# Optimization experiments

Hardware: AMD Instinct MI355X
Metric: run time of the kernel (lower is better)

Reference implementation:

```python
import jax, jax.numpy as jnp
import numpy as np

ALPHA_SCALE = 8.0  # exp(alpha_log_scale) where alpha_log_scale = log(8)
EPS = 1e-6


def _depthwise_causal_conv(x, conv_w, conv_b):
    # x: [N, H, T], conv_w: [H, 1, K], conv_b: [H]
    K = conv_w.shape[-1]
    y = jax.lax.conv_general_dilated(
        x, conv_w,
        window_strides=(1,),
        padding=[(K - 1, 0)],  # causal: torch pads both sides then slices [..., :T]
        dimension_numbers=("NCH", "OIH", "NCH"),
        feature_group_count=x.shape[1],
    )
    return y + conv_b[None, :, None]


def _linear_scan(alpha, x):
    # h_t = alpha_t * h_{t-1} + x_t along time axis=1; alpha, x: [N, T, H]
    def combine(c1, c2):
        a1, b1 = c1
        a2, b2 = c2
        return a1 * a2, a2 * b1 + b2
    _, h = jax.lax.associative_scan(combine, (alpha, x), axis=1)
    return h


def setup_inputs() -> dict:
    key = jax.random.key(0)
    ks = jax.random.split(key, 8)
    N, T, D = 4, 4096, 1024
    H, K = 1536, 4
    return {
        "x": jax.random.normal(ks[0], (N, T, D), dtype=jnp.float32),
        "W_in": jax.random.normal(ks[1], (2 * H, D), dtype=jnp.float32) * (D ** -0.5),
        "conv_w": jax.random.normal(ks[2], (H, 1, K), dtype=jnp.float32) * 0.1,
        "conv_b": jax.random.normal(ks[3], (H,), dtype=jnp.float32) * 0.1,
        "W_g": jax.random.normal(ks[4], (2 * H, H), dtype=jnp.float32) * (H ** -0.5),
        "b_g": jax.random.normal(ks[5], (2 * H,), dtype=jnp.float32) * 0.1,
        "forget_base": jax.random.normal(ks[6], (H,), dtype=jnp.float32),
        "W_out": jax.random.normal(ks[7], (D, H), dtype=jnp.float32) * (H ** -0.5),
    }


def reference(x, W_in, conv_w, conv_b, W_g, b_g, forget_base, W_out):
    H = W_g.shape[1]
    # input projection and split into gate / x branch
    gx = jnp.einsum("ntd,hd->nth", x, W_in)  # [N,T,2H]
    gate, xb = gx[..., :H], gx[..., H:]
    # depthwise causal conv
    xb = _depthwise_causal_conv(jnp.swapaxes(xb, 1, 2), conv_w, conv_b)
    xb = jnp.swapaxes(xb, 1, 2)  # [N,T,H]
    # gates
    fg = jnp.einsum("nth,gh->ntg", xb, W_g) + b_g  # [N,T,2H]
    forget, inp = fg[..., :H], fg[..., H:]
    # RG-LRU gating
    alpha = jnp.exp(-ALPHA_SCALE * jax.nn.softplus(forget_base) * jax.nn.sigmoid(forget))
    beta = jnp.sqrt(1.0 - alpha ** 2 + EPS)
    xs = beta * jax.nn.sigmoid(inp) * xb
    # linear recurrence h_t = alpha_t * h_{t-1} + xs_t
    h = _linear_scan(alpha, xs)
    # output projection with GeLU-gated hidden state (torch gelu = exact erf form)
    return jnp.einsum("nth,dh->ntd", jax.nn.gelu(gate, approximate=False) * h, W_out)
```

## Files before the change

### kernel.cpp

```cpp
#include <hip/hip_runtime.h>
#include <stdint.h>
#include <math.h>

#define N_B 4
#define T_S 4096
#define D_M 1024
#define H_M 1536
#define NT  (N_B * T_S)
#define G2  (2 * H_M)
#define LCH 64
#define NCH 64

typedef __attribute__((ext_vector_type(8))) short short8;
typedef __attribute__((ext_vector_type(4))) float floatx4;

__device__ __forceinline__ unsigned short f2bf(float f) {
  unsigned u = __float_as_uint(f);
  u += 0x7fff + ((u >> 16) & 1);
  return (unsigned short)(u >> 16);
}
__device__ __forceinline__ float bf2f(unsigned short u) {
  return __uint_as_float(((unsigned)u) << 16);
}
__device__ __forceinline__ float bf_lo(unsigned p) { return __uint_as_float(p << 16); }
__device__ __forceinline__ float bf_hi(unsigned p) { return __uint_as_float(p & 0xffff0000u); }
__device__ __forceinline__ unsigned bf_pack(float lo, float hi) {
  return ((unsigned)f2bf(lo)) | (((unsigned)f2bf(hi)) << 16);
}
__device__ __forceinline__ float sigmoidf_(float x) { return 1.f / (1.f + __expf(-x)); }
__device__ __forceinline__ float softplusf_(float x) {
  return (x > 20.f) ? x : log1pf(__expf(x));
}
__device__ __forceinline__ float geluf_(float x) {
  return 0.5f * x * (1.f + erff(x * 0.70710678118654752f));
}

__global__ void zero_out(float* __restrict__ out, int n) {
  int i = blockIdx.x * 256 + threadIdx.x;
  if (i < n) out[i] = 0.f;
}

#define N4_X   (NT * D_M / 4)
#define N4_WIN (G2 * D_M / 4)
#define N4_WG  (G2 * H_M / 4)
__global__ void cvt3_bf16(const float* __restrict__ x, unsigned short* __restrict__ x16,
                          const float* __restrict__ win, unsigned short* __restrict__ win16,
                          const float* __restrict__ wg, unsigned short* __restrict__ wg16) {
  int i = blockIdx.x * 256 + threadIdx.x;
  const float* in; unsigned short* out;
  if (i < N4_X)                { in = x;   out = x16; }
  else if (i < N4_X + N4_WIN)  { in = win; out = win16; i -= N4_X; }
  else if (i < N4_X + N4_WIN + N4_WG) { in = wg; out = wg16; i -= N4_X + N4_WIN; }
  else return;
  float4 v = ((const float4*)in)[i];
  ushort4 o;
  o.x = f2bf(v.x); o.y = f2bf(v.y); o.z = f2bf(v.z); o.w = f2bf(v.w);
  ((ushort4*)out)[i] = o;
}

__global__ void cvt_bf16(const float* __restrict__ in, unsigned short* __restrict__ out, int n4) {
  int i = blockIdx.x * 256 + threadIdx.x;
  if (i >= n4) return;
  float4 v = ((const float4*)in)[i];
  ushort4 o;
  o.x = f2bf(v.x); o.y = f2bf(v.y); o.z = f2bf(v.z); o.w = f2bf(v.w);
  ((ushort4*)out)[i] = o;
}

#define TM 256
#define TN 256

__device__ __forceinline__ void stage16(const unsigned short* g, unsigned short* l) {
  __builtin_amdgcn_global_load_lds((__attribute__((address_space(1))) void*)g,
                                   (__attribute__((address_space(3))) void*)l, 16, 0, 0);
}

template<bool BIAS, bool OUT_BF16, bool SPLIT>
__global__ __launch_bounds__(512, 2)
void gemm_bt8(const unsigned short* __restrict__ A,
              const unsigned short* __restrict__ B,
              void* __restrict__ Cv, void* __restrict__ Cv2,
              const float* __restrict__ bias,
              int N, int K) {
  __shared__ __align__(16) unsigned short lds[4][8192];
  const int tid  = threadIdx.x;
  const int lane = tid & 63;
  const int wave = tid >> 6;
  const int wr = wave >> 2;
  const int wc = wave & 3;

  const int gx  = gridDim.x;
  const int nwg = gx * gridDim.y;
  const int bid = blockIdx.y * gx + blockIdx.x;
  const int cpx = nwg >> 3;
  const int swz = (bid & 7) * cpx + (bid >> 3);
  const int bm = (swz / gx) * TM;
  const int bn = (swz % gx) * TN;

  floatx4 acc[8][4];
#pragma unroll
  for (int i = 0; i < 8; i++)
#pragma unroll
    for (int j = 0; j < 4; j++)
      acc[i][j] = (floatx4){0.f, 0.f, 0.f, 0.f};

  const int r0_ = tid >> 2;
  const int g8  = ((tid & 3) ^ ((tid >> 3) & 3)) * 8;
  const unsigned short* Ag1 = A + (size_t)(bm + r0_)       * K + g8;
  const unsigned short* Ag2 = A + (size_t)(bm + r0_ + 128) * K + g8;
  const unsigned short* Bg1 = B + (size_t)(bn + r0_)       * K + g8;
  const unsigned short* Bg2 = B + (size_t)(bn + r0_ + 128) * K + g8;
  const int ld1 = tid * 8;
  const int ld2 = ld1 + 4096;

#define STAGE_A(kh, kb) do { \
    stage16(Ag1 + (kb) + (kh) * 32, &lds[kh][ld1]); \
    stage16(Ag2 + (kb) + (kh) * 32, &lds[kh][ld2]); } while (0)
#define STAGE_B(kh, kb) do { \
    stage16(Bg1 + (kb) + (kh) * 32, &lds[2 + (kh)][ld1]); \
    stage16(Bg2 + (kb) + (kh) * 32, &lds[2 + (kh)][ld2]); } while (0)

  const int fr = lane & 15;
  const int kq = lane >> 4;
  const int sx = (kq ^ ((fr >> 1) & 3)) * 8;
  const int abase = (wr * 128 + fr) * 32 + sx;
  const int bbase = (wc * 64 + fr) * 32 + sx;

  const int nt = K >> 6;
  short8 af[8], bfr[2];

  STAGE_A(0, 0); STAGE_B(0, 0); STAGE_A(1, 0);

  for (int t = 0; t < nt; ++t) {
    const int k0 = t << 6;
    const int kn = k0 + 64;
    const bool st = (t + 1 < nt);

    STAGE_B(1, k0);
    asm volatile("s_waitcnt vmcnt(4)" ::: "memory");
    __builtin_amdgcn_s_barrier();
#pragma unroll
    for (int i = 0; i < 8; ++i) af[i]  = *(const short8*)(&lds[0][abase + i * 512]);
#pragma unroll
    for (int j = 0; j < 2; ++j) bfr[j] = *(const short8*)(&lds[2][bbase + j * 512]);
    __builtin_amdgcn_s_setprio(1);
#pragma unroll
    for (int i = 0; i < 8; ++i)
#pragma unroll
      for (int j = 0; j < 2; ++j)
        acc[i][j] = __builtin_amdgcn_mfma_f32_16x16x32_bf16(af[i], bfr[j], acc[i][j], 0, 0, 0);
    __builtin_amdgcn_s_setprio(0);
    __builtin_amdgcn_s_barrier();

    if (st) STAGE_A(0, kn);
#pragma unroll
    for (int j = 0; j < 2; ++j) bfr[j] = *(const short8*)(&lds[2][bbase + 1024 + j * 512]);
    __builtin_amdgcn_s_setprio(1);
#pragma unroll
    for (int i = 0; i < 8; ++i)
#pragma unroll
      for (int j = 0; j < 2; ++j)
        acc[i][2 + j] = __builtin_amdgcn_mfma_f32_16x16x32_bf16(af[i], bfr[j], acc[i][2 + j], 0, 0, 0);
    __builtin_amdgcn_s_setprio(0);
    __builtin_amdgcn_s_barrier();

    if (st) STAGE_B(0, kn);
    if (st) { asm volatile("s_waitcnt vmcnt(4)" ::: "memory"); }
    else    { asm volatile("s_waitcnt vmcnt(0)" ::: "memory"); }
    __builtin_amdgcn_s_barrier();
#pragma unroll
    for (int i = 0; i < 8; ++i) af[i]  = *(const short8*)(&lds[1][abase + i * 512]);
#pragma unroll
    for (int j = 0; j < 2; ++j) bfr[j] = *(const short8*)(&lds[3][bbase + j * 512]);
    __builtin_amdgcn_s_setprio(1);
#pragma unroll
    for (int i = 0; i < 8; ++i)
#pragma unroll
      for (int j = 0; j < 2; ++j)
        acc[i][j] = __builtin_amdgcn_mfma_f32_16x16x32_bf16(af[i], bfr[j], acc[i][j], 0, 0, 0);
    __builtin_amdgcn_s_setprio(0);
    __builtin_amdgcn_s_barrier();

    if (st) STAGE_A(1, kn);
#pragma unroll
    for (int j = 0; j < 2; ++j) bfr[j] = *(const short8*)(&lds[3][bbase + 1024 + j * 512]);
    __builtin_amdgcn_s_setprio(1);
#pragma unroll
    for (int i = 0; i < 8; ++i)
#pragma unroll
      for (int j = 0; j < 2; ++j)
        acc[i][2 + j] = __builtin_amdgcn_mfma_f32_16x16x32_bf16(af[i], bfr[j], acc[i][2 + j], 0, 0, 0);
    __builtin_amdgcn_s_setprio(0);
    __builtin_amdgcn_s_barrier();
  }
#undef STAGE_A
#undef STAGE_B

  const int half  = SPLIT ? (N >> 1) : N;
  const bool hi   = SPLIT && (bn >= half);
  void* Cb        = hi ? Cv2 : Cv;
  const int coff  = hi ? half : 0;
  const int cn = lane & 15;
  const int rb = (lane >> 4) * 4;
  float bv[4];
#pragma unroll
  for (int j = 0; j < 4; ++j)
    bv[j] = BIAS ? bias[bn + wc * 64 + j * 16 + cn] : 0.f;
  const int col0 = bn + wc * 64 + cn - coff;
#pragma unroll
  for (int i = 0; i < 8; ++i) {
    const int row0 = bm + wr * 128 + i * 16 + rb;
#pragma unroll
    for (int r = 0; r < 4; ++r) {
      const size_t rowb = (size_t)(row0 + r) * half + col0;
#pragma unroll
      for (int j = 0; j < 4; ++j) {
        float v = acc[i][j][r] + bv[j];
        if (OUT_BF16) ((unsigned short*)Cb)[rowb + j * 16] = f2bf(v);
        else          ((float*)Cb)[rowb + j * 16] = v;
      }
    }
  }
}

__global__ void conv_dw(const unsigned int* __restrict__ xbpre2, const float* __restrict__ cw,
                        const float* __restrict__ cb, unsigned int* __restrict__ xbc2) {
  int i0 = blockIdx.x * 256 + threadIdx.x;
  int t = blockIdx.y;
  size_t nt = (size_t)blockIdx.z * T_S + t;
  const int h = 2 * i0;
  const float4 wa = ((const float4*)cw)[h];
  const float4 wb = ((const float4*)cw)[h + 1];
  const float2 cb2 = ((const float2*)cb)[i0];
  size_t base = nt * (H_M / 2) + i0;
  unsigned p0 = xbpre2[base];
  float aa = cb2.x + wa.w * bf_lo(p0);
  float ab = cb2.y + wb.w * bf_hi(p0);
  if (t >= 1) { unsigned p = xbpre2[base - H_M / 2];
    aa += wa.z * bf_lo(p); ab += wb.z * bf_hi(p); }
  if (t >= 2) { unsigned p = xbpre2[base - 2 * (size_t)(H_M / 2)];
    aa += wa.y * bf_lo(p); ab += wb.y * bf_hi(p); }
  if (t >= 3) { unsigned p = xbpre2[base - 3 * (size_t)(H_M / 2)];
    aa += wa.x * bf_lo(p); ab += wb.x * bf_hi(p); }
  xbc2[base] = bf_pack(aa, ab);
}

__global__ void scan_A(const unsigned int* __restrict__ fg2, const unsigned int* __restrict__ xbc2,
                       const float* __restrict__ fb,
                       float2* __restrict__ cA2, float2* __restrict__ cS2) {
  int i0 = blockIdx.x * 256 + threadIdx.x;
  int ch = blockIdx.y;
  int n = blockIdx.z;
  const float2 fb2 = ((const float2*)fb)[i0];
  const float c8a = 8.f * softplusf_(fb2.x);
  const float c8b = 8.f * softplusf_(fb2.y);
  float apa = 1.f, sa = 0.f, apb = 1.f, sb = 0.f;
  size_t r = (size_t)n * T_S + (size_t)ch * LCH;
  for (int i = 0; i < LCH; i++, r++) {
    unsigned pf = fg2[r * (G2 / 2) + i0];
    unsigned pi = fg2[r * (G2 / 2) + H_M / 2 + i0];
    unsigned px = xbc2[r * (H_M / 2) + i0];
    float alpha_a = __expf(-c8a * sigmoidf_(bf_lo(pf)));
    float alpha_b = __expf(-c8b * sigmoidf_(bf_hi(pf)));
    float beta_a = sqrtf(1.f - alpha_a * alpha_a + 1e-6f);
    float beta_b = sqrtf(1.f - alpha_b * alpha_b + 1e-6f);
    sa = alpha_a * sa + beta_a * sigmoidf_(bf_lo(pi)) * bf_lo(px);
    sb = alpha_b * sb + beta_b * sigmoidf_(bf_hi(pi)) * bf_hi(px);
    apa *= alpha_a;
    apb *= alpha_b;
  }
  size_t o = ((size_t)n * NCH + ch) * (H_M / 2) + i0;
  cA2[o] = make_float2(apa, apb);
  cS2[o] = make_float2(sa, sb);
}

__global__ void scan_C(const unsigned int* __restrict__ fg2, const unsigned int* __restrict__ xbc2,
                       const float* __restrict__ fb,
                       const float2* __restrict__ cA2, const float2* __restrict__ cS2,
                       unsigned int* gateh2) {
  int i0 = blockIdx.x * 256 + threadIdx.x;
  int ch = blockIdx.y;
  int n = blockIdx.z;
  const float2 fb2 = ((const float2*)fb)[i0];
  const float c8a = 8.f * softplusf_(fb2.x);
  const float c8b = 8.f * softplusf_(fb2.y);
  float sa = 0.f, sb = 0.f;
  for (int c = 0; c < ch; c++) {
    size_t o = ((size_t)n * NCH + c) * (H_M / 2) + i0;
    float2 a = cA2[o], s = cS2[o];
    sa = a.x * sa + s.x;
    sb = a.y * sb + s.y;
  }
  size_t r = (size_t)n * T_S + (size_t)ch * LCH;
  for (int i = 0; i < LCH; i++, r++) {
    unsigned pf = fg2[r * (G2 / 2) + i0];
    unsigned pi = fg2[r * (G2 / 2) + H_M / 2 + i0];
    unsigned px = xbc2[r * (H_M / 2) + i0];
    float alpha_a = __expf(-c8a * sigmoidf_(bf_lo(pf)));
    float alpha_b = __expf(-c8b * sigmoidf_(bf_hi(pf)));
    float beta_a = sqrtf(1.f - alpha_a * alpha_a + 1e-6f);
    float beta_b = sqrtf(1.f - alpha_b * alpha_b + 1e-6f);
    sa = alpha_a * sa + beta_a * sigmoidf_(bf_lo(pi)) * bf_lo(px);
    sb = alpha_b * sb + beta_b * sigmoidf_(bf_hi(pi)) * bf_hi(px);
    unsigned pg = gateh2[r * (H_M / 2) + i0];
    gateh2[r * (H_M / 2) + i0] = bf_pack(geluf_(bf_lo(pg)) * sa, geluf_(bf_hi(pg)) * sb);
  }
}

extern "C" void kernel_launch(void* const* d_in, const int* in_sizes, int n_in,
                              void* d_out, int out_size, void* d_ws, size_t ws_size,
                              hipStream_t stream) {
  const float* x    = (const float*)d_in[0];
  const float* Win  = (const float*)d_in[1];
  const float* cw   = (const float*)d_in[2];
  const float* cb   = (const float*)d_in[3];
  const float* Wg   = (const float*)d_in[4];
  const float* bg   = (const float*)d_in[5];
  const float* fb   = (const float*)d_in[6];
  const float* Wout = (const float*)d_in[7];
  float* out = (float*)d_out;
  (void)in_sizes; (void)n_in;

  const size_t S = (size_t)NT * H_M * 2;
  const size_t needed = 4 * S + (size_t)G2 * H_M * 2;
  if (ws_size < needed) {
    zero_out<<<(out_size + 255) / 256, 256, 0, stream>>>(out, out_size);
    return;
  }

  char* base = (char*)d_ws;
  unsigned short* gate16  = (unsigned short*)(base);
  unsigned short* xbpre16 = (unsigned short*)(base + S);
  unsigned short* fg16    = (unsigned short*)(base + S);
  unsigned short* x16     = (unsigned short*)(base + 2 * S);
  unsigned short* Win16   = (unsigned short*)(base + 2 * S + (size_t)NT * D_M * 2);
  unsigned short* xbc16   = (unsigned short*)(base + 3 * S);
  unsigned short* Wg16    = (unsigned short*)(base + 4 * S);
  float* cA    = (float*)(base + 4 * S);
  float* cS    = cA + (size_t)N_B * NCH * H_M;
  unsigned short* Wout16  = (unsigned short*)(cS + (size_t)N_B * NCH * H_M);

  cvt3_bf16<<<(N4_X + N4_WIN + N4_WG + 255) / 256, 256, 0, stream>>>(
      x, x16, Win, Win16, Wg, Wg16);

  gemm_bt8<false, true, true><<<dim3(G2 / TN, NT / TM), 512, 0, stream>>>(
      x16, Win16, gate16, xbpre16, nullptr, G2, D_M);
  conv_dw<<<dim3(H_M / 512, T_S, N_B), 256, 0, stream>>>(
      (const unsigned int*)xbpre16, cw, cb, (unsigned int*)xbc16);
  gemm_bt8<true, true, false><<<dim3(G2 / TN, NT / TM), 512, 0, stream>>>(
      xbc16, Wg16, fg16, nullptr, bg, G2, H_M);
  cvt_bf16<<<(D_M * H_M / 4 + 255) / 256, 256, 0, stream>>>(Wout, Wout16, D_M * H_M / 4);
  scan_A<<<dim3(H_M / 512, NCH, N_B), 256, 0, stream>>>(
      (const unsigned int*)fg16, (const unsigned int*)xbc16, fb, (float2*)cA, (float2*)cS);
  scan_C<<<dim3(H_M / 512, NCH, N_B), 256, 0, stream>>>(
      (const unsigned int*)fg16, (const unsigned int*)xbc16, fb,
      (const float2*)cA, (const float2*)cS, (unsigned int*)gate16);
  gemm_bt8<false, false, false><<<dim3(D_M / TN, NT / TM), 512, 0, stream>>>(
      gate16, Wout16, out, nullptr, nullptr, D_M, H_M);
}
```

Before: 645.2 us.

## Double-buffer LDS in bf16 GEMM to prefetch next K tile during MFMA

```diff
diff --git a/kernel.cpp b/kernel.cpp
--- a/kernel.cpp
+++ b/kernel.cpp
@@ -82,7 +82,7 @@
               void* __restrict__ Cv, void* __restrict__ Cv2,
               const float* __restrict__ bias,
               int N, int K) {
-  __shared__ __align__(16) unsigned short lds[4][8192];
+  __shared__ __align__(16) unsigned short lds[2][4][8192];
   const int tid  = threadIdx.x;
   const int lane = tid & 63;
   const int wave = tid >> 6;
@@ -113,12 +113,12 @@
   const int ld1 = tid * 8;
   const int ld2 = ld1 + 4096;
 
-#define STAGE_A(kh, kb) do { \
-    stage16(Ag1 + (kb) + (kh) * 32, &lds[kh][ld1]); \
-    stage16(Ag2 + (kb) + (kh) * 32, &lds[kh][ld2]); } while (0)
-#define STAGE_B(kh, kb) do { \
-    stage16(Bg1 + (kb) + (kh) * 32, &lds[2 + (kh)][ld1]); \
-    stage16(Bg2 + (kb) + (kh) * 32, &lds[2 + (kh)][ld2]); } while (0)
+#define STAGE_A(bu, kh, kb) do { \
+    stage16(Ag1 + (kb) + (kh) * 32, &lds[bu][kh][ld1]); \
+    stage16(Ag2 + (kb) + (kh) * 32, &lds[bu][kh][ld2]); } while (0)
+#define STAGE_B(bu, kh, kb) do { \
+    stage16(Bg1 + (kb) + (kh) * 32, &lds[bu][2 + (kh)][ld1]); \
+    stage16(Bg2 + (kb) + (kh) * 32, &lds[bu][2 + (kh)][ld2]); } while (0)
 
   const int fr = lane & 15;
   const int kq = lane >> 4;
@@ -127,22 +127,25 @@
   const int bbase = (wc * 64 + fr) * 32 + sx;
 
   const int nt = K >> 6;
-  short8 af[8], bfr[2];
-
-  STAGE_A(0, 0); STAGE_B(0, 0); STAGE_A(1, 0);
+  short8 af[8], bfr[4];
+
+  STAGE_A(0, 0, 0); STAGE_B(0, 0, 0); STAGE_A(0, 1, 0); STAGE_B(0, 1, 0);
+  asm volatile("s_waitcnt vmcnt(4)" ::: "memory");
+  __builtin_amdgcn_s_barrier();
 
   for (int t = 0; t < nt; ++t) {
-    const int k0 = t << 6;
-    const int kn = k0 + 64;
+    const int d  = t & 1;
+    const int dn = d ^ 1;
+    const int kn = (t + 1) << 6;
     const bool st = (t + 1 < nt);
 
-    STAGE_B(1, k0);
-    asm volatile("s_waitcnt vmcnt(4)" ::: "memory");
-    __builtin_amdgcn_s_barrier();
-#pragma unroll
-    for (int i = 0; i < 8; ++i) af[i]  = *(const short8*)(&lds[0][abase + i * 512]);
-#pragma unroll
-    for (int j = 0; j < 2; ++j) bfr[j] = *(const short8*)(&lds[2][bbase + j * 512]);
+#pragma unroll
+    for (int i = 0; i < 8; ++i) af[i]  = *(const short8*)(&lds[d][0][abase + i * 512]);
+#pragma unroll
+    for (int j = 0; j < 4; ++j) bfr[j] = *(const short8*)(&lds[d][2][bbase + j * 512]);
+    if (st) STAGE_A(dn, 0, kn);
+    __builtin_amdgcn_s_barrier();
+    asm volatile("s_waitcnt lgkmcnt(0)" ::: "memory");
     __builtin_amdgcn_s_setprio(1);
 #pragma unroll
     for (int i = 0; i < 8; ++i)
@@ -152,26 +155,26 @@
     __builtin_amdgcn_s_setprio(0);
     __builtin_amdgcn_s_barrier();
 
-    if (st) STAGE_A(0, kn);
-#pragma unroll
-    for (int j = 0; j < 2; ++j) bfr[j] = *(const short8*)(&lds[2][bbase + 1024 + j * 512]);
-    __builtin_amdgcn_s_setprio(1);
-#pragma unroll
-    for (int i = 0; i < 8; ++i)
-#pragma unroll
-      for (int j = 0; j < 2; ++j)
-        acc[i][2 + j] = __builtin_amdgcn_mfma_f32_16x16x32_bf16(af[i], bfr[j], acc[i][2 + j], 0, 0, 0);
-    __builtin_amdgcn_s_setprio(0);
-    __builtin_amdgcn_s_barrier();
-
-    if (st) STAGE_B(0, kn);
+    if (st) STAGE_B(dn, 0, kn);
     if (st) { asm volatile("s_waitcnt vmcnt(4)" ::: "memory"); }
     else    { asm volatile("s_waitcnt vmcnt(0)" ::: "memory"); }
     __builtin_amdgcn_s_barrier();
-#pragma unroll
-    for (int i = 0; i < 8; ++i) af[i]  = *(const short8*)(&lds[1][abase + i * 512]);
-#pragma unroll
-    for (int j = 0; j < 2; ++j) bfr[j] = *(const short8*)(&lds[3][bbase + j * 512]);
+    __builtin_amdgcn_s_setprio(1);
+#pragma unroll
+    for (int i = 0; i < 8; ++i)
+#pragma unroll
+      for (int j = 0; j < 2; ++j)
+        acc[i][2 + j] = __builtin_amdgcn_mfma_f32_16x16x32_bf16(af[i], bfr[2 + j], acc[i][2 + j], 0, 0, 0);
+    __builtin_amdgcn_s_setprio(0);
+    __builtin_amdgcn_s_barrier();
+
+#pragma unroll
+    for (int i = 0; i < 8; ++i) af[i]  = *(const short8*)(&lds[d][1][abase + i * 512]);
+#pragma unroll
+    for (int j = 0; j < 4; ++j) bfr[j] = *(const short8*)(&lds[d][3][bbase + j * 512]);
+    if (st) STAGE_A(dn, 1, kn);
+    __builtin_amdgcn_s_barrier();
+    asm volatile("s_waitcnt lgkmcnt(0)" ::: "memory");
     __builtin_amdgcn_s_setprio(1);
 #pragma unroll
     for (int i = 0; i < 8; ++i)
@@ -181,15 +184,15 @@
     __builtin_amdgcn_s_setprio(0);
     __builtin_amdgcn_s_barrier();
 
-    if (st) STAGE_A(1, kn);
-#pragma unroll
-    for (int j = 0; j < 2; ++j) bfr[j] = *(const short8*)(&lds[3][bbase + 1024 + j * 512]);
+    if (st) STAGE_B(dn, 1, kn);
+    if (st) { asm volatile("s_waitcnt vmcnt(4)" ::: "memory"); }
+    __builtin_amdgcn_s_barrier();
     __builtin_amdgcn_s_setprio(1);
 #pragma unroll
     for (int i = 0; i < 8; ++i)
 #pragma unroll
       for (int j = 0; j < 2; ++j)
-        acc[i][2 + j] = __builtin_amdgcn_mfma_f32_16x16x32_bf16(af[i], bfr[j], acc[i][2 + j], 0, 0, 0);
+        acc[i][2 + j] = __builtin_amdgcn_mfma_f32_16x16x32_bf16(af[i], bfr[2 + j], acc[i][2 + j], 0, 0, 0);
     __builtin_amdgcn_s_setprio(0);
     __builtin_amdgcn_s_barrier();
   }
```

After: 676.7 us. 4.9% more time.

## Double-buffer GEMM LDS tiles with 64-wide K rows and fewer barriers

Applied to the files above, without the earlier changes.

```diff
diff --git a/kernel.cpp b/kernel.cpp
--- a/kernel.cpp
+++ b/kernel.cpp
@@ -82,7 +82,8 @@
               void* __restrict__ Cv, void* __restrict__ Cv2,
               const float* __restrict__ bias,
               int N, int K) {
-  __shared__ __align__(16) unsigned short lds[4][8192];
+  __shared__ __align__(16) unsigned short As[2][2][8192];
+  __shared__ __align__(16) unsigned short Bs[2][2][8192];
   const int tid  = threadIdx.x;
   const int lane = tid & 63;
   const int wave = tid >> 6;
@@ -104,94 +105,124 @@
     for (int j = 0; j < 4; j++)
       acc[i][j] = (floatx4){0.f, 0.f, 0.f, 0.f};
 
-  const int r0_ = tid >> 2;
-  const int g8  = ((tid & 3) ^ ((tid >> 3) & 3)) * 8;
-  const unsigned short* Ag1 = A + (size_t)(bm + r0_)       * K + g8;
-  const unsigned short* Ag2 = A + (size_t)(bm + r0_ + 128) * K + g8;
-  const unsigned short* Bg1 = B + (size_t)(bn + r0_)       * K + g8;
-  const unsigned short* Bg2 = B + (size_t)(bn + r0_ + 128) * K + g8;
-  const int ld1 = tid * 8;
-  const int ld2 = ld1 + 4096;
-
-#define STAGE_A(kh, kb) do { \
-    stage16(Ag1 + (kb) + (kh) * 32, &lds[kh][ld1]); \
-    stage16(Ag2 + (kb) + (kh) * 32, &lds[kh][ld2]); } while (0)
-#define STAGE_B(kh, kb) do { \
-    stage16(Bg1 + (kb) + (kh) * 32, &lds[2 + (kh)][ld1]); \
-    stage16(Bg2 + (kb) + (kh) * 32, &lds[2 + (kh)][ld2]); } while (0)
+  const int r0_ = tid >> 3;
+  const int g8  = ((tid & 7) ^ (r0_ & 7)) * 8;
+  const unsigned short* Ag[2][2];
+  const unsigned short* Bg[2][2];
+#pragma unroll
+  for (int h = 0; h < 2; ++h)
+#pragma unroll
+    for (int u = 0; u < 2; ++u) {
+      Ag[h][u] = A + (size_t)(bm + h * 128 + r0_ + 64 * u) * K + g8;
+      Bg[h][u] = B + (size_t)(bn + h * 128 + r0_ + 64 * u) * K + g8;
+    }
+  const int ldd = tid * 8;
+
+#define STAGE_A(bu, h, kb) do { \
+    stage16(Ag[h][0] + (kb), &As[bu][h][ldd]); \
+    stage16(Ag[h][1] + (kb), &As[bu][h][ldd + 4096]); } while (0)
+#define STAGE_B(bu, h, kb) do { \
+    stage16(Bg[h][0] + (kb), &Bs[bu][h][ldd]); \
+    stage16(Bg[h][1] + (kb), &Bs[bu][h][ldd + 4096]); } while (0)
 
   const int fr = lane & 15;
   const int kq = lane >> 4;
-  const int sx = (kq ^ ((fr >> 1) & 3)) * 8;
-  const int abase = (wr * 128 + fr) * 32 + sx;
-  const int bbase = (wc * 64 + fr) * 32 + sx;
+  const int e8 = fr & 7;
+  const int px0 = (kq ^ e8) * 8;
+  const int px1 = ((4 + kq) ^ e8) * 8;
+  const int arow = fr * 64;
+  const int brow = ((wc & 1) * 64 + fr) * 64;
 
   const int nt = K >> 6;
-  short8 af[8], bfr[2];
-
-  STAGE_A(0, 0); STAGE_B(0, 0); STAGE_A(1, 0);
+  short8 af[2][2], bfr[4][2];
+
+  STAGE_A(0, 0, 0); STAGE_A(0, 1, 0);
+  STAGE_B(0, 0, 0); STAGE_B(0, 1, 0);
+  if (nt > 1) { STAGE_B(1, 0, 64); STAGE_B(1, 1, 64); }
 
   for (int t = 0; t < nt; ++t) {
-    const int k0 = t << 6;
-    const int kn = k0 + 64;
-    const bool st = (t + 1 < nt);
-
-    STAGE_B(1, k0);
-    asm volatile("s_waitcnt vmcnt(4)" ::: "memory");
+    const int par = t & 1;
+    const int kn1 = (t + 1) << 6;
+    const int kn2 = (t + 2) << 6;
+    const bool s1 = (t + 1 < nt);
+    const bool s2 = (t + 2 < nt);
+
+    if (s1) { asm volatile("s_waitcnt vmcnt(4)" ::: "memory"); }
+    else    { asm volatile("s_waitcnt vmcnt(0)" ::: "memory"); }
     __builtin_amdgcn_s_barrier();
-#pragma unroll
-    for (int i = 0; i < 8; ++i) af[i]  = *(const short8*)(&lds[0][abase + i * 512]);
-#pragma unroll
-    for (int j = 0; j < 2; ++j) bfr[j] = *(const short8*)(&lds[2][bbase + j * 512]);
+
+    const unsigned short* Ab = &As[par][wr][0];
+    const unsigned short* Bb = &Bs[par][wc >> 1][0];
+
+#pragma unroll
+    for (int j = 0; j < 4; ++j) {
+      bfr[j][0] = *(const short8*)(Bb + brow + j * 1024 + px0);
+      bfr[j][1] = *(const short8*)(Bb + brow + j * 1024 + px1);
+    }
+#pragma unroll
+    for (int ii = 0; ii < 2; ++ii) {
+      af[ii][0] = *(const short8*)(Ab + arow + ii * 1024 + px0);
+      af[ii][1] = *(const short8*)(Ab + arow + ii * 1024 + px1);
+    }
+    if (s1) STAGE_A(par ^ 1, 0, kn1);
     __builtin_amdgcn_s_setprio(1);
 #pragma unroll
-    for (int i = 0; i < 8; ++i)
-#pragma unroll
-      for (int j = 0; j < 2; ++j)
-        acc[i][j] = __builtin_amdgcn_mfma_f32_16x16x32_bf16(af[i], bfr[j], acc[i][j], 0, 0, 0);
+    for (int kh = 0; kh < 2; ++kh)
+#pragma unroll
+      for (int ii = 0; ii < 2; ++ii)
+#pragma unroll
+        for (int j = 0; j < 4; ++j)
+          acc[ii][j] = __builtin_amdgcn_mfma_f32_16x16x32_bf16(af[ii][kh], bfr[j][kh], acc[ii][j], 0, 0, 0);
     __builtin_amdgcn_s_setprio(0);
     __builtin_amdgcn_s_barrier();
 
-    if (st) STAGE_A(0, kn);
-#pragma unroll
-    for (int j = 0; j < 2; ++j) bfr[j] = *(const short8*)(&lds[2][bbase + 1024 + j * 512]);
+#pragma unroll
+    for (int ii = 0; ii < 2; ++ii) {
+      af[ii][0] = *(const short8*)(Ab + arow + (2048 + ii * 1024) + px0);
+      af[ii][1] = *(const short8*)(Ab + arow + (2048 + ii * 1024) + px1);
+    }
+    if (s1) STAGE_A(par ^ 1, 1, kn1);
+    if (s2) STAGE_B(par, 0, kn2);
     __builtin_amdgcn_s_setprio(1);
 #pragma unroll
-    for (int i = 0; i < 8; ++i)
-#pragma unroll
-      for (int j = 0; j < 2; ++j)
-        acc[i][2 + j] = __builtin_amdgcn_mfma_f32_16x16x32_bf16(af[i], bfr[j], acc[i][2 + j], 0, 0, 0);
+    for (int kh = 0; kh < 2; ++kh)
+#pragma unroll
+      for (int ii = 0; ii < 2; ++ii)
+#pragma unroll
+        for (int j = 0; j < 4; ++j)
+          acc[2 + ii][j] = __builtin_amdgcn_mfma_f32_16x16x32_bf16(af[ii][kh], bfr[j][kh], acc[2 + ii][j], 0, 0, 0);
     __builtin_amdgcn_s_setprio(0);
-    __builtin_amdgcn_s_barrier();
-
-    if (st) STAGE_B(0, kn);
-    if (st) { asm volatile("s_waitcnt vmcnt(4)" ::: "memory"); }
-    else    { asm volatile("s_waitcnt vmcnt(0)" ::: "memory"); }
-    __builtin_amdgcn_s_barrier();
-#pragma unroll
-    for (int i = 0; i < 8; ++i) af[i]  = *(const short8*)(&lds[1][abase + i * 512]);
-#pragma unroll
-    for (int j = 0; j < 2; ++j) bfr[j] = *(const short8*)(&lds[3][bbase + j * 512]);
+
+#pragma unroll
+    for (int ii = 0; ii < 2; ++ii) {
+      af[ii][0] = *(const short8*)(Ab + arow + (4096 + ii * 1024) + px0);
+      af[ii][1] = *(const short8*)(Ab + arow + (4096 + ii * 1024) + px1);
+    }
+    if (s2) STAGE_B(par, 1, kn2);
     __builtin_amdgcn_s_setprio(1);
 #pragma unroll
-    for (int i = 0; i < 8; ++i)
-#pragma unroll
-      for (int j = 0; j < 2; ++j)
-        acc[i][j] = __builtin_amdgcn_mfma_f32_16x16x32_bf16(af[i], bfr[j], acc[i][j], 0, 0, 0);
+    for (int kh = 0; kh < 2; ++kh)
+#pragma unroll
+      for (int ii = 0; ii < 2; ++ii)
+#pragma unroll
+        for (int j = 0; j < 4; ++j)
+          acc[4 + ii][j] = __builtin_amdgcn_mfma_f32_16x16x32_bf16(af[ii][kh], bfr[j][kh], acc[4 + ii][j], 0, 0, 0);
     __builtin_amdgcn_s_setprio(0);
-    __builtin_amdgcn_s_barrier();
-
-    if (st) STAGE_A(1, kn);
-#pragma unroll
-    for (int j = 0; j < 2; ++j) bfr[j] = *(const short8*)(&lds[3][bbase + 1024 + j * 512]);
+
+#pragma unroll
+    for (int ii = 0; ii < 2; ++ii) {
+      af[ii][0] = *(const short8*)(Ab + arow + (6144 + ii * 1024) + px0);
+      af[ii][1] = *(const short8*)(Ab + arow + (6144 + ii * 1024) + px1);
+    }
     __builtin_amdgcn_s_setprio(1);
 #pragma unroll
-    for (int i = 0; i < 8; ++i)
-#pragma unroll
-      for (int j = 0; j < 2; ++j)
-        acc[i][2 + j] = __builtin_amdgcn_mfma_f32_16x16x32_bf16(af[i], bfr[j], acc[i][2 + j], 0, 0, 0);
+    for (int kh = 0; kh < 2; ++kh)
+#pragma unroll
+      for (int ii = 0; ii < 2; ++ii)
+#pragma unroll
+        for (int j = 0; j < 4; ++j)
+          acc[6 + ii][j] = __builtin_amdgcn_mfma_f32_16x16x32_bf16(af[ii][kh], bfr[j][kh], acc[6 + ii][j], 0, 0, 0);
     __builtin_amdgcn_s_setprio(0);
-    __builtin_amdgcn_s_barrier();
   }
 #undef STAGE_A
 #undef STAGE_B
```

New measurement: 655.7 us. About the same (+1.6%).
